# Kernel optimization log

Measured on AMD Instinct MI355X. Metric: run time of the kernel, lower is better.

Reference implementation:

```python
import jax, jax.numpy as jnp
import numpy as np

MARGIN = 0.2
N = 512
D = 128
N_CLASSES = 64


def setup_inputs() -> dict:
    key = jax.random.key(0)
    k1, k2 = jax.random.split(key)
    z = jax.random.normal(k1, (N, D), dtype=jnp.float32)
    labels = jax.random.randint(k2, (N,), 0, N_CLASSES)
    return {"z": z, "labels": labels}


def _pdist(x, y):
    sq = (jnp.sum(x * x, axis=1)[:, None]
          + jnp.sum(y * y, axis=1)[None, :]
          - 2.0 * (x @ y.T))
    sq = jnp.maximum(sq, 0.0)
    pos = sq > 0
    # safe sqrt (diagonal is exactly 0; avoid inf gradient there)
    return jnp.sqrt(jnp.where(pos, sq, 1.0)) * pos


def reference(z, labels):
    n = labels.shape[0]
    d = _pdist(z, z)                                  # [N, N]
    same = labels[None, :] == labels[:, None]         # [N, N]
    diff = ~same
    same = same & ~jnp.eye(n, dtype=bool)             # fill_diagonal_(False)
    # valid triplet mask [anchor, pos, neg]
    mask = same[:, :, None] & diff[:, None, :]        # [N, N, N] bool
    # d(a,p) - d(a,n) + margin over all (a,p,n)
    losses = d[:, :, None] - d[:, None, :] + MARGIN   # [N, N, N]
    n_eg = jnp.sum((losses > 0) & mask)
    n_triplets = jnp.sum(mask).astype(losses.dtype)
    loss = jnp.sum(jnp.where(mask, jax.nn.relu(losses), 0.0)) / n_triplets
    return loss, n_eg
```

## Files before the change

kernel.cpp:

```cpp
#include <hip/hip_runtime.h>

#define NPTS 512
#define DIM 128
#define MARGIN 0.2f
#define ATILE 2
#define NBLK (NPTS / ATILE)
#define TROWS 256
#define NTILE (NPTS / TROWS)
#define NTHR 512

__global__ __launch_bounds__(NTHR) void triplet_partial_kernel(
    const float* __restrict__ z, const int* __restrict__ labels,
    float* __restrict__ psum, unsigned* __restrict__ pcnt,
    unsigned* __restrict__ pntrip)
{
    __shared__ float4 stage[TROWS * 32];
    __shared__ float part[4][TROWS][ATILE];
    __shared__ float drow[ATILE][NPTS];
    __shared__ __align__(16) float pdm[ATILE][NPTS];
    __shared__ int wcnt[ATILE][8];
    __shared__ float red_f[8];
    __shared__ unsigned red_c[8];

    const int t = threadIdx.x;
    const int b = blockIdx.x;
    const int a0 = b * ATILE;
    const int wid = t >> 6, lane = t & 63;
    const int q = t >> 7;
    const int r = t & 127;

    const float4* zg = reinterpret_cast<const float4*>(z);

    float4 za[ATILE][8];
    #pragma unroll
    for (int i = 0; i < ATILE; ++i)
        #pragma unroll
        for (int kk = 0; kk < 8; ++kk)
            za[i][kk] = zg[(size_t)(a0 + i) * 32 + q * 8 + kk];

    for (int T = 0; T < NTILE; ++T) {
        #pragma unroll
        for (int p = 0; p < 16; ++p) {
            int f = p * 512 + t;
            int row = f >> 5, chunk = f & 31;
            stage[row * 32 + (chunk ^ (row & 7))] =
                zg[(size_t)(T * TROWS + row) * 32 + chunk];
        }
        __syncthreads();

        #pragma unroll
        for (int rr = 0; rr < 2; ++rr) {
            const int row = r + rr * 128;
            const int rx = row & 7;
            float acc0 = 0.f, acc1 = 0.f;
            #pragma unroll
            for (int kk = 0; kk < 8; ++kk) {
                float4 v = stage[row * 32 + ((q * 8 + kk) ^ rx)];
                float4 w0 = za[0][kk], w1 = za[1][kk];
                float d0 = w0.x - v.x, d1 = w0.y - v.y, d2 = w0.z - v.z, d3 = w0.w - v.w;
                acc0 += d0 * d0 + d1 * d1 + d2 * d2 + d3 * d3;
                float e0 = w1.x - v.x, e1 = w1.y - v.y, e2 = w1.z - v.z, e3 = w1.w - v.w;
                acc1 += e0 * e0 + e1 * e1 + e2 * e2 + e3 * e3;
            }
            part[q][row][0] = acc0;
            part[q][row][1] = acc1;
        }
        __syncthreads();

        {
            const int rr = t & 255, ii = t >> 8;
            float s = part[0][rr][ii] + part[1][rr][ii]
                    + part[2][rr][ii] + part[3][rr][ii];
            drow[ii][T * TROWS + rr] = sqrtf(s);
        }
    }
    __syncthreads();

    const int lt = labels[t];
    int la[ATILE];
    #pragma unroll
    for (int i = 0; i < ATILE; ++i) la[i] = labels[a0 + i];

    bool pred[ATILE];
    unsigned long long m[ATILE];
    #pragma unroll
    for (int i = 0; i < ATILE; ++i) {
        pred[i] = (lt == la[i]) && (t != a0 + i);
        m[i] = __ballot(pred[i]);
        if (lane == 0) wcnt[i][wid] = (int)__popcll(m[i]);
    }
    __syncthreads();

    unsigned np[ATILE], npad[ATILE];
    #pragma unroll
    for (int i = 0; i < ATILE; ++i) {
        unsigned base = 0, n = 0;
        #pragma unroll
        for (int w = 0; w < 8; ++w) {
            unsigned c = (unsigned)wcnt[i][w];
            if (w < wid) base += c;
            n += c;
        }
        np[i] = n;
        npad[i] = (n + 3u) & ~3u;
        if (pred[i])
            pdm[i][base + __popcll(m[i] & ((1ull << lane) - 1ull))] = drow[i][t] + MARGIN;
        if ((unsigned)t >= n && (unsigned)t < npad[i])
            pdm[i][t] = -1e30f;
    }
    __syncthreads();

    float sum = 0.f;
    unsigned cnt = 0;
    #pragma unroll
    for (int i = 0; i < ATILE; ++i) {
        if (lt != la[i]) {
            const float si = drow[i][t];
            const float4* p4 = reinterpret_cast<const float4*>(pdm[i]);
            const int n4 = (int)(npad[i] >> 2);
            for (int p = 0; p < n4; ++p) {
                float4 qv = p4[p];
                float v0 = qv.x - si, v1 = qv.y - si, v2 = qv.z - si, v3 = qv.w - si;
                if (v0 > 0.f) { sum += v0; ++cnt; }
                if (v1 > 0.f) { sum += v1; ++cnt; }
                if (v2 > 0.f) { sum += v2; ++cnt; }
                if (v3 > 0.f) { sum += v3; ++cnt; }
            }
        }
    }

    #pragma unroll
    for (int off = 32; off > 0; off >>= 1) {
        sum += __shfl_down(sum, off, 64);
        cnt += __shfl_down(cnt, off, 64);
    }
    if (lane == 0) { red_f[wid] = sum; red_c[wid] = cnt; }
    __syncthreads();
    if (t == 0) {
        float S = 0.f;
        unsigned C = 0;
        #pragma unroll
        for (int w = 0; w < 8; ++w) { S += red_f[w]; C += red_c[w]; }
        unsigned NT = 0;
        #pragma unroll
        for (int i = 0; i < ATILE; ++i) NT += np[i] * (unsigned)(NPTS - 1 - np[i]);
        psum[b] = S;
        pcnt[b] = C;
        pntrip[b] = NT;
    }
}

__global__ __launch_bounds__(256) void triplet_final_kernel(
    const float* __restrict__ psum, const unsigned* __restrict__ pcnt,
    const unsigned* __restrict__ pntrip, float* __restrict__ out)
{
    __shared__ float rf[4];
    __shared__ unsigned rc[4], rn[4];

    const int t = threadIdx.x;
    float s = psum[t];
    unsigned c = pcnt[t];
    unsigned nt = pntrip[t];

    #pragma unroll
    for (int off = 32; off > 0; off >>= 1) {
        s  += __shfl_down(s,  off, 64);
        c  += __shfl_down(c,  off, 64);
        nt += __shfl_down(nt, off, 64);
    }
    const int wid = t >> 6, lane = t & 63;
    if (lane == 0) { rf[wid] = s; rc[wid] = c; rn[wid] = nt; }
    __syncthreads();
    if (t == 0) {
        double S = 0.0;
        unsigned C = 0, NT = 0;
        #pragma unroll
        for (int w = 0; w < 4; ++w) { S += (double)rf[w]; C += rc[w]; NT += rn[w]; }
        out[0] = (float)(S / (double)NT);
        out[1] = (float)C;
    }
}

extern "C" void kernel_launch(void* const* d_in, const int* in_sizes, int n_in,
                              void* d_out, int out_size, void* d_ws, size_t ws_size,
                              hipStream_t stream) {
    const float* z = (const float*)d_in[0];
    const int* labels = (const int*)d_in[1];
    float* out = (float*)d_out;

    float* psum = (float*)d_ws;
    unsigned* pcnt = (unsigned*)((char*)d_ws + NBLK * sizeof(float));
    unsigned* pntrip = pcnt + NBLK;

    triplet_partial_kernel<<<NBLK, NTHR, 0, stream>>>(z, labels, psum, pcnt, pntrip);
    triplet_final_kernel<<<1, NBLK, 0, stream>>>(psum, pcnt, pntrip, out);
}
```

Baseline: 15.08 us.

## Merge final reduction into partial kernel via cooperative grid sync

Replaces the two-kernel launch with one cooperative kernel. All blocks write their partials, a grid-wide sync follows, and block 0 then does the final reduction. This removes a second kernel launch and the gap between launches. The cost is a cooperative launch, which needs all 256 blocks resident at once, plus the grid-barrier overhead.

Result: slower. 44.65 us (+196.1%).

```diff
diff --git a/kernel.cpp b/kernel.cpp
--- a/kernel.cpp
+++ b/kernel.cpp
@@ -1,4 +1,7 @@
 #include <hip/hip_runtime.h>
+#include <hip/hip_cooperative_groups.h>
+
+namespace cg = cooperative_groups;
 
 #define NPTS 512
 #define DIM 128
@@ -9,10 +12,10 @@
 #define NTILE (NPTS / TROWS)
 #define NTHR 512
 
-__global__ __launch_bounds__(NTHR) void triplet_partial_kernel(
+__global__ __launch_bounds__(NTHR) void triplet_coop_kernel(
     const float* __restrict__ z, const int* __restrict__ labels,
     float* __restrict__ psum, unsigned* __restrict__ pcnt,
-    unsigned* __restrict__ pntrip)
+    unsigned* __restrict__ pntrip, float* __restrict__ out)
 {
     __shared__ float4 stage[TROWS * 32];
     __shared__ float part[4][TROWS][ATILE];
@@ -20,7 +23,7 @@
     __shared__ __align__(16) float pdm[ATILE][NPTS];
     __shared__ int wcnt[ATILE][8];
     __shared__ float red_f[8];
-    __shared__ unsigned red_c[8];
+    __shared__ unsigned red_c[8], red_n[8];
 
     const int t = threadIdx.x;
     const int b = blockIdx.x;
@@ -148,36 +151,33 @@
         pcnt[b] = C;
         pntrip[b] = NT;
     }
-}
 
-__global__ __launch_bounds__(256) void triplet_final_kernel(
-    const float* __restrict__ psum, const unsigned* __restrict__ pcnt,
-    const unsigned* __restrict__ pntrip, float* __restrict__ out)
-{
-    __shared__ float rf[4];
-    __shared__ unsigned rc[4], rn[4];
+    cg::this_grid().sync();
 
-    const int t = threadIdx.x;
-    float s = psum[t];
-    unsigned c = pcnt[t];
-    unsigned nt = pntrip[t];
-
-    #pragma unroll
-    for (int off = 32; off > 0; off >>= 1) {
-        s  += __shfl_down(s,  off, 64);
-        c  += __shfl_down(c,  off, 64);
-        nt += __shfl_down(nt, off, 64);
-    }
-    const int wid = t >> 6, lane = t & 63;
-    if (lane == 0) { rf[wid] = s; rc[wid] = c; rn[wid] = nt; }
-    __syncthreads();
-    if (t == 0) {
-        double S = 0.0;
-        unsigned C = 0, NT = 0;
+    if (b == 0) {
+        float s = 0.f;
+        unsigned c = 0, nt = 0;
+        if (t < NBLK) {
+            s = psum[t]; c = pcnt[t]; nt = pntrip[t];
+        }
         #pragma unroll
-        for (int w = 0; w < 4; ++w) { S += (double)rf[w]; C += rc[w]; NT += rn[w]; }
-        out[0] = (float)(S / (double)NT);
-        out[1] = (float)C;
+        for (int off = 32; off > 0; off >>= 1) {
+            s  += __shfl_down(s,  off, 64);
+            c  += __shfl_down(c,  off, 64);
+            nt += __shfl_down(nt, off, 64);
+        }
+        if (lane == 0) { red_f[wid] = s; red_c[wid] = c; red_n[wid] = nt; }
+        __syncthreads();
+        if (t == 0) {
+            double S = 0.0;
+            unsigned C = 0, NT = 0;
+            #pragma unroll
+            for (int w = 0; w < 4; ++w) {
+                S += (double)red_f[w]; C += red_c[w]; NT += red_n[w];
+            }
+            out[0] = (float)(S / (double)NT);
+            out[1] = (float)C;
+        }
     }
 }
 
@@ -192,6 +192,8 @@
     unsigned* pcnt = (unsigned*)((char*)d_ws + NBLK * sizeof(float));
     unsigned* pntrip = pcnt + NBLK;
 
-    triplet_partial_kernel<<<NBLK, NTHR, 0, stream>>>(z, labels, psum, pcnt, pntrip);
-    triplet_final_kernel<<<1, NBLK, 0, stream>>>(psum, pcnt, pntrip, out);
+    void* args[] = { (void*)&z, (void*)&labels, (void*)&psum,
+                     (void*)&pcnt, (void*)&pntrip, (void*)&out };
+    hipLaunchCooperativeKernel((void*)triplet_coop_kernel,
+                               dim3(NBLK), dim3(NTHR), args, 0, stream);
 }
```
